# Kernel optimization log

Measured on AMD Instinct MI355X. Metric: run time of the kernel, lower is better.

The kernel has to match this reference:

```python
import jax, jax.numpy as jnp
import numpy as np

GS = 128      # quantization group size along K (in_features)
EPS = 1e-8

def setup_inputs() -> dict:
    key = jax.random.key(0)
    k1, k2, k3, k4 = jax.random.split(key, 4)
    B, S, K, N = 4, 2048, 4096, 4096
    x = jax.random.normal(k1, (B, S, K), dtype=jnp.float32)
    weight = jax.random.normal(k2, (N, K), dtype=jnp.float32) * 0.02   # torch Linear layout [out, in]
    bias = jax.random.normal(k3, (N,), dtype=jnp.float32) * 0.01
    # per-group (K//gs) x per-out-channel quant steps, strictly positive
    step_scales = jax.random.uniform(k4, (K // GS, N), dtype=jnp.float32, minval=0.01, maxval=0.05)
    return {"x": x, "weight": weight, "bias": bias, "step_scales": step_scales}

def reference(x, weight, bias, step_scales):
    # w: [K, N] (forward transposes the Linear weight)
    w = weight.T
    K, N = w.shape
    G = K // GS
    wg = w.reshape(G, GS, N)                       # group along K
    s = step_scales[:, None, :] + EPS              # [G, 1, N]
    # group-quantized dequant: round-to-step per (group, out-channel)
    q = jnp.round(wg / s)
    w_dq = (q * s).reshape(K, N)
    out = jnp.einsum('bsk,kn->bsn', x, w_dq)
    if bias is not None:
        out = out + bias
    return out
```

## Files before the change

### kernel.cpp

```cpp
#include <hip/hip_runtime.h>
#include <hip/hip_bf16.h>
#include <stdint.h>

typedef unsigned short u16;
typedef __bf16 bf16x8 __attribute__((ext_vector_type(8)));
typedef float f32x4 __attribute__((ext_vector_type(4)));
typedef unsigned short u16x8 __attribute__((ext_vector_type(8)));

#define QEPS 1e-8f

__device__ __forceinline__ u16 f32_to_bf16_rne(float f) {
    uint32_t u = __float_as_uint(f);
    u += 0x7fffu + ((u >> 16) & 1u);
    return (u16)(u >> 16);
}

__global__ void cvt_x_bf16(const float* __restrict__ x, u16* __restrict__ xb, int n8) {
    int idx = blockIdx.x * blockDim.x + threadIdx.x;
    if (idx >= n8) return;
    const float4* p = (const float4*)(x + (size_t)idx * 8);
    float4 a = p[0], b = p[1];
    u16x8 r;
    r[0] = f32_to_bf16_rne(a.x); r[1] = f32_to_bf16_rne(a.y);
    r[2] = f32_to_bf16_rne(a.z); r[3] = f32_to_bf16_rne(a.w);
    r[4] = f32_to_bf16_rne(b.x); r[5] = f32_to_bf16_rne(b.y);
    r[6] = f32_to_bf16_rne(b.z); r[7] = f32_to_bf16_rne(b.w);
    *(u16x8*)(xb + (size_t)idx * 8) = r;
}

__global__ void dequant_w_bf16(const float* __restrict__ w, const float* __restrict__ ss,
                               u16* __restrict__ wb, int N, int K) {
    int idx = blockIdx.x * blockDim.x + threadIdx.x;
    int pr = K >> 3;
    if (idx >= N * pr) return;
    int n = idx / pr;
    int k8 = (idx - n * pr) << 3;
    float s = ss[(size_t)(k8 >> 7) * N + n] + QEPS;
    const float4* p = (const float4*)(w + (size_t)n * K + k8);
    float4 a = p[0], b = p[1];
    float v[8] = {a.x, a.y, a.z, a.w, b.x, b.y, b.z, b.w};
    u16x8 r;
#pragma unroll
    for (int i = 0; i < 8; ++i) {
        float q = rintf(v[i] / s);
        r[i] = f32_to_bf16_rne(q * s);
    }
    *(u16x8*)(wb + (size_t)n * K + k8) = r;
}

#define BM 256
#define BN 256
#define BK 32
#define BUFB 32768
#define ABYT 16384
#define LDSB 131072

#define ASYNC16(g, l)                                                                      \
    __builtin_amdgcn_global_load_lds((const __attribute__((address_space(1))) void*)(g),   \
                                     (__attribute__((address_space(3))) void*)(l), 16, 0, 0)
#define VMCNT(n) asm volatile("s_waitcnt vmcnt(" #n ")" ::: "memory")

__global__ __launch_bounds__(512, 2) void gemm_bf16_bt_256(
        const u16* __restrict__ A,
        const u16* __restrict__ B,
        const float* __restrict__ bias,
        float* __restrict__ C,
        int M, int N, int K) {
    extern __shared__ char lds[];
    const int tid  = threadIdx.x;
    const int wave = tid >> 6;
    const int lane = tid & 63;

    const int nwg = gridDim.x;
    const int cpx = nwg >> 3;
    const int bid = blockIdx.x;
    const int swz = (bid & 7) * cpx + (bid >> 3);
    const int nbn = N / BN;
    const int bm  = swz / nbn;
    const int bn  = swz - bm * nbn;

    const int wr = wave >> 2;
    const int wc = wave & 3;

    const int srow  = tid >> 2;
    const int kbsrc = ((tid & 3) << 4) ^ (((tid >> 3) & 3) << 4);
    const char* gA0 = (const char*)A + ((size_t)(bm * BM + srow) * K) * 2 + kbsrc;
    const char* gA1 = (const char*)A + ((size_t)(bm * BM + 128 + srow) * K) * 2 + kbsrc;
    const char* gB0 = (const char*)B + ((size_t)(bn * BN + srow) * K) * 2 + kbsrc;
    const char* gB1 = (const char*)B + ((size_t)(bn * BN + 128 + srow) * K) * 2 + kbsrc;
    char* ldsw = lds + (wave << 10);

    auto STAGE = [&](int t) {
        const size_t ko = (size_t)t << 6;
        char* d = ldsw + ((t & 3) * BUFB);
        ASYNC16(gA0 + ko, d);
        ASYNC16(gA1 + ko, d + 8192);
        ASYNC16(gB0 + ko, d + ABYT);
        ASYNC16(gB1 + ko, d + ABYT + 8192);
    };

    const int kx = ((lane >> 4) ^ ((lane >> 1) & 3)) << 4;
    const char* pa = lds + (size_t)(wr * 128 + (lane & 15)) * 64 + kx;
    const char* pb = lds + ABYT + (size_t)(wc * 64 + (lane & 15)) * 64 + kx;

    f32x4 acc[8][4] = {};

    auto COMPUTE = [&](int t) {
        const int bo = (t & 3) * BUFB;
        bf16x8 bfr[4], af[8];
#pragma unroll
        for (int n = 0; n < 4; ++n) bfr[n] = *(const bf16x8*)(pb + bo + n * 1024);
#pragma unroll
        for (int m = 0; m < 8; ++m) af[m] = *(const bf16x8*)(pa + bo + m * 1024);
        __builtin_amdgcn_s_setprio(1);
#pragma unroll
        for (int m = 0; m < 8; ++m)
#pragma unroll
            for (int n = 0; n < 4; ++n)
                acc[m][n] = __builtin_amdgcn_mfma_f32_16x16x32_bf16(af[m], bfr[n], acc[m][n], 0, 0, 0);
        __builtin_amdgcn_s_setprio(0);
    };

    const int NT = K >> 5;

    STAGE(0); STAGE(1); STAGE(2);
    VMCNT(8);
    __builtin_amdgcn_s_barrier();

    for (int t = 0; t < NT - 3; ++t) {
        STAGE(t + 3);
        COMPUTE(t);
        VMCNT(8);
        __builtin_amdgcn_s_barrier();
    }
    COMPUTE(NT - 3); VMCNT(4); __builtin_amdgcn_s_barrier();
    COMPUTE(NT - 2); VMCNT(0); __builtin_amdgcn_s_barrier();
    COMPUTE(NT - 1);

    const int r0 = bm * BM + wr * 128 + ((lane >> 4) << 2);
    const int c0 = bn * BN + wc * 64 + (lane & 15);
    float bv[4];
#pragma unroll
    for (int n = 0; n < 4; ++n) bv[n] = bias[c0 + n * 16];
#pragma unroll
    for (int m = 0; m < 8; ++m)
#pragma unroll
        for (int n = 0; n < 4; ++n)
#pragma unroll
            for (int i = 0; i < 4; ++i)
                C[(size_t)(r0 + m * 16 + i) * N + (c0 + n * 16)] = acc[m][n][i] + bv[n];
}

extern "C" void kernel_launch(void* const* d_in, const int* in_sizes, int n_in,
                              void* d_out, int out_size, void* d_ws, size_t ws_size,
                              hipStream_t stream) {
    const float* x    = (const float*)d_in[0];
    const float* w    = (const float*)d_in[1];
    const float* bias = (const float*)d_in[2];
    const float* ss   = (const float*)d_in[3];
    float* out        = (float*)d_out;

    const int N = in_sizes[2];
    const int K = in_sizes[1] / N;
    const int M = in_sizes[0] / K;

    u16* xb = (u16*)d_ws;
    u16* wb = xb + (size_t)M * K;

    int n8x = (M * K) >> 3;
    cvt_x_bf16<<<(n8x + 255) / 256, 256, 0, stream>>>(x, xb, n8x);

    int n8w = (N * K) >> 3;
    dequant_w_bf16<<<(n8w + 255) / 256, 256, 0, stream>>>(w, ss, wb, N, K);

    (void)hipFuncSetAttribute((const void*)gemm_bf16_bt_256,
                              hipFuncAttributeMaxDynamicSharedMemorySize, LDSB);
    dim3 grid((M / BM) * (N / BN));
    gemm_bf16_bt_256<<<grid, 512, LDSB, stream>>>(xb, wb, bias, out, M, N, K);
}
```

Baseline: 281.3 us.

## Split GEMM main loop into two interleaved LDS-load/MFMA phases with staged prefetch

Splits each K-step of the bf16 GEMM main loop into two half-phases. Each phase issues half the A-fragment LDS reads, one half of the async global-to-LDS prefetch (A then B), a barrier and an lgkmcnt wait, then half the MFMAs. The intent is to interleave LDS reads, global prefetch and MFMA work more finely across waves, ping-pong style. It adds two extra barriers per iteration, which can cost more than the overlap gains.

```diff
diff --git a/kernel.cpp b/kernel.cpp
--- a/kernel.cpp
+++ b/kernel.cpp
@@ -59,6 +59,8 @@
     __builtin_amdgcn_global_load_lds((const __attribute__((address_space(1))) void*)(g),   \
                                      (__attribute__((address_space(3))) void*)(l), 16, 0, 0)
 #define VMCNT(n) asm volatile("s_waitcnt vmcnt(" #n ")" ::: "memory")
+#define LGKM0()  do { asm volatile("s_waitcnt lgkmcnt(0)" ::: "memory");                   \
+                      __builtin_amdgcn_sched_barrier(0); } while (0)
 
 __global__ __launch_bounds__(512, 2) void gemm_bf16_bt_256(
         const u16* __restrict__ A,
@@ -90,11 +92,15 @@
     const char* gB1 = (const char*)B + ((size_t)(bn * BN + 128 + srow) * K) * 2 + kbsrc;
     char* ldsw = lds + (wave << 10);
 
-    auto STAGE = [&](int t) {
+    auto STAGE_A = [&](int t) {
         const size_t ko = (size_t)t << 6;
         char* d = ldsw + ((t & 3) * BUFB);
         ASYNC16(gA0 + ko, d);
         ASYNC16(gA1 + ko, d + 8192);
+    };
+    auto STAGE_B = [&](int t) {
+        const size_t ko = (size_t)t << 6;
+        char* d = ldsw + ((t & 3) * BUFB);
         ASYNC16(gB0 + ko, d + ABYT);
         ASYNC16(gB1 + ko, d + ABYT + 8192);
     };
@@ -123,13 +129,39 @@
 
     const int NT = K >> 5;
 
-    STAGE(0); STAGE(1); STAGE(2);
+    STAGE_A(0); STAGE_B(0); STAGE_A(1); STAGE_B(1); STAGE_A(2); STAGE_B(2);
     VMCNT(8);
     __builtin_amdgcn_s_barrier();
 
     for (int t = 0; t < NT - 3; ++t) {
-        STAGE(t + 3);
-        COMPUTE(t);
+        const int bo = (t & 3) * BUFB;
+        bf16x8 bfr[4], af[8];
+#pragma unroll
+        for (int n = 0; n < 4; ++n) bfr[n] = *(const bf16x8*)(pb + bo + n * 1024);
+#pragma unroll
+        for (int m = 0; m < 4; ++m) af[m] = *(const bf16x8*)(pa + bo + m * 1024);
+        STAGE_A(t + 3);
+        __builtin_amdgcn_s_barrier();
+        LGKM0();
+        __builtin_amdgcn_s_setprio(1);
+#pragma unroll
+        for (int m = 0; m < 4; ++m)
+#pragma unroll
+            for (int n = 0; n < 4; ++n)
+                acc[m][n] = __builtin_amdgcn_mfma_f32_16x16x32_bf16(af[m], bfr[n], acc[m][n], 0, 0, 0);
+        __builtin_amdgcn_s_setprio(0);
+#pragma unroll
+        for (int m = 4; m < 8; ++m) af[m] = *(const bf16x8*)(pa + bo + m * 1024);
+        STAGE_B(t + 3);
+        __builtin_amdgcn_s_barrier();
+        LGKM0();
+        __builtin_amdgcn_s_setprio(1);
+#pragma unroll
+        for (int m = 4; m < 8; ++m)
+#pragma unroll
+            for (int n = 0; n < 4; ++n)
+                acc[m][n] = __builtin_amdgcn_mfma_f32_16x16x32_bf16(af[m], bfr[n], acc[m][n], 0, 0, 0);
+        __builtin_amdgcn_s_setprio(0);
         VMCNT(8);
         __builtin_amdgcn_s_barrier();
     }
```

Result: no change. 285.5 us (+1.5%).

## Split GEMM main loop into two half-phases with register prefetch of next tile

Applied to the files above, without the earlier changes.

Restructures the bf16 GEMM main loop so each K-step runs as two MFMA halves (rows 0-3 and 4-7). A and B global-to-LDS staging is split across the halves, and the next tile's B and low-A fragments are prefetched from LDS into registers during the second half. The goal is to overlap LDS reads and global async loads with MFMA work and to interleave waves with extra barriers and schedule fences. The cost is more barriers per iteration and more live registers, which could hurt occupancy at two waves per SIMD. It also relies on delicate vmcnt accounting and buffer reuse ordering.

```diff
diff --git a/kernel.cpp b/kernel.cpp
--- a/kernel.cpp
+++ b/kernel.cpp
@@ -50,8 +50,7 @@
 
 #define BM 256
 #define BN 256
-#define BK 32
-#define BUFB 32768
+#define SLOTB 32768
 #define ABYT 16384
 #define LDSB 131072
 
@@ -59,6 +58,8 @@
     __builtin_amdgcn_global_load_lds((const __attribute__((address_space(1))) void*)(g),   \
                                      (__attribute__((address_space(3))) void*)(l), 16, 0, 0)
 #define VMCNT(n) asm volatile("s_waitcnt vmcnt(" #n ")" ::: "memory")
+#define SBAR()   __builtin_amdgcn_sched_barrier(0)
+#define BAR()    __builtin_amdgcn_s_barrier()
 
 __global__ __launch_bounds__(512, 2) void gemm_bf16_bt_256(
         const u16* __restrict__ A,
@@ -88,15 +89,18 @@
     const char* gA1 = (const char*)A + ((size_t)(bm * BM + 128 + srow) * K) * 2 + kbsrc;
     const char* gB0 = (const char*)B + ((size_t)(bn * BN + srow) * K) * 2 + kbsrc;
     const char* gB1 = (const char*)B + ((size_t)(bn * BN + 128 + srow) * K) * 2 + kbsrc;
-    char* ldsw = lds + (wave << 10);
-
-    auto STAGE = [&](int t) {
+
+    auto stageA = [&](int t) {
         const size_t ko = (size_t)t << 6;
-        char* d = ldsw + ((t & 3) * BUFB);
+        char* d = lds + ((t & 3) * SLOTB) + (wave << 10);
         ASYNC16(gA0 + ko, d);
         ASYNC16(gA1 + ko, d + 8192);
-        ASYNC16(gB0 + ko, d + ABYT);
-        ASYNC16(gB1 + ko, d + ABYT + 8192);
+    };
+    auto stageB = [&](int t) {
+        const size_t ko = (size_t)t << 6;
+        char* d = lds + ((t & 3) * SLOTB) + ABYT + (wave << 10);
+        ASYNC16(gB0 + ko, d);
+        ASYNC16(gB1 + ko, d + 8192);
     };
 
     const int kx = ((lane >> 4) ^ ((lane >> 1) & 3)) << 4;
@@ -104,38 +108,62 @@
     const char* pb = lds + ABYT + (size_t)(wc * 64 + (lane & 15)) * 64 + kx;
 
     f32x4 acc[8][4] = {};
-
-    auto COMPUTE = [&](int t) {
-        const int bo = (t & 3) * BUFB;
-        bf16x8 bfr[4], af[8];
-#pragma unroll
-        for (int n = 0; n < 4; ++n) bfr[n] = *(const bf16x8*)(pb + bo + n * 1024);
-#pragma unroll
-        for (int m = 0; m < 8; ++m) af[m] = *(const bf16x8*)(pa + bo + m * 1024);
-        __builtin_amdgcn_s_setprio(1);
-#pragma unroll
-        for (int m = 0; m < 8; ++m)
-#pragma unroll
-            for (int n = 0; n < 4; ++n)
-                acc[m][n] = __builtin_amdgcn_mfma_f32_16x16x32_bf16(af[m], bfr[n], acc[m][n], 0, 0, 0);
-        __builtin_amdgcn_s_setprio(0);
-    };
-
-    const int NT = K >> 5;
-
-    STAGE(0); STAGE(1); STAGE(2);
+    bf16x8 rB[4], rA0[4], rA1[4], rB2[4], rA02[4];
+
+#define MFMA16_LO()                                                           \
+    _Pragma("unroll") for (int m = 0; m < 4; ++m)                             \
+    _Pragma("unroll") for (int n = 0; n < 4; ++n)                             \
+        acc[m][n] = __builtin_amdgcn_mfma_f32_16x16x32_bf16(rA0[m], rB[n], acc[m][n], 0, 0, 0);
+#define MFMA16_HI()                                                           \
+    _Pragma("unroll") for (int m = 0; m < 4; ++m)                             \
+    _Pragma("unroll") for (int n = 0; n < 4; ++n)                             \
+        acc[m + 4][n] = __builtin_amdgcn_mfma_f32_16x16x32_bf16(rA1[m], rB[n], acc[m + 4][n], 0, 0, 0);
+
+#define UNIT_BODY(u, VMSTMT, DO_STAGE, DO_PREF)                               \
+    {                                                                         \
+        const int sb  = ((u) & 3) * SLOTB;                                    \
+        const int sb1 = (((u) + 1) & 3) * SLOTB;                              \
+                                     \
+        _Pragma("unroll") for (int m = 0; m < 4; ++m)                         \
+            rA1[m] = *(const bf16x8*)(pa + sb + (m + 4) * 1024);              \
+        if (DO_STAGE) stageA((u) + 3);                                        \
+        VMSTMT;                                                               \
+        SBAR(); BAR(); SBAR();                                                \
+        __builtin_amdgcn_s_setprio(1);                                        \
+        MFMA16_LO();                                                          \
+        __builtin_amdgcn_s_setprio(0);                                        \
+        BAR();                                                                \
+                 \
+        if (DO_PREF) {                                                        \
+            _Pragma("unroll") for (int n = 0; n < 4; ++n)                     \
+                rB2[n] = *(const bf16x8*)(pb + sb1 + n * 1024);               \
+            _Pragma("unroll") for (int m = 0; m < 4; ++m)                     \
+                rA02[m] = *(const bf16x8*)(pa + sb1 + m * 1024);              \
+        }                                                                     \
+        if (DO_STAGE) stageB((u) + 3);                                        \
+        SBAR(); BAR(); SBAR();                                                \
+        __builtin_amdgcn_s_setprio(1);                                        \
+        MFMA16_HI();                                                          \
+        __builtin_amdgcn_s_setprio(0);                                        \
+        BAR();                                                                \
+        _Pragma("unroll") for (int i = 0; i < 4; ++i) { rB[i] = rB2[i]; rA0[i] = rA02[i]; } \
+    }
+
+    const int NU = K >> 5;
+
+    stageA(0); stageB(0); stageA(1); stageB(1); stageA(2); stageB(2);
     VMCNT(8);
-    __builtin_amdgcn_s_barrier();
-
-    for (int t = 0; t < NT - 3; ++t) {
-        STAGE(t + 3);
-        COMPUTE(t);
-        VMCNT(8);
-        __builtin_amdgcn_s_barrier();
-    }
-    COMPUTE(NT - 3); VMCNT(4); __builtin_amdgcn_s_barrier();
-    COMPUTE(NT - 2); VMCNT(0); __builtin_amdgcn_s_barrier();
-    COMPUTE(NT - 1);
+    BAR();
+#pragma unroll
+    for (int n = 0; n < 4; ++n) rB[n] = *(const bf16x8*)(pb + n * 1024);
+#pragma unroll
+    for (int m = 0; m < 4; ++m) rA0[m] = *(const bf16x8*)(pa + m * 1024);
+
+    for (int u = 0; u < NU - 3; ++u)
+        UNIT_BODY(u, VMCNT(6), true, true);
+    UNIT_BODY(NU - 3, VMCNT(4), false, true);
+    UNIT_BODY(NU - 2, VMCNT(0), false, true);
+    UNIT_BODY(NU - 1, (void)0, false, false);
 
     const int r0 = bm * BM + wr * 128 + ((lane >> 4) << 2);
     const int c0 = bn * BN + wc * 64 + (lane & 15);
```

Result: slower. 296.3 us (+5.3%).
